# Performance work log

Measured on AMD Instinct MI355X. Metric: run time of the kernel, lower is better.

The kernel has to match this reference:

```python
import jax, jax.numpy as jnp
import numpy as np

B, C_IN, C_OUT, H, W = 4, 256, 256, 64, 64
KH = KW = 3
STRIDE = 1
PAD = 1
DIL = 1


def setup_inputs() -> dict:
    key = jax.random.key(0)
    k1, k2, k3, k4 = jax.random.split(key, 4)
    x = jax.random.normal(k1, (B, C_IN, H, W), dtype=jnp.float32)
    # torchvision layout: 2*dg*KH*KW channels, (y, x) pair per kernel tap
    offset = jax.random.normal(k2, (B, 2 * KH * KW, H, W), dtype=jnp.float32)
    fan_in = C_IN * KH * KW
    weight = jax.random.normal(k3, (C_OUT, C_IN, KH, KW), dtype=jnp.float32) / np.sqrt(fan_in)
    bias = jax.random.normal(k4, (C_OUT,), dtype=jnp.float32) * 0.01
    return {"x": x, "offset": offset, "weight": weight, "bias": bias}


def _gather_bilinear_corner(x_flat, yi, xi, h, w):
    # x_flat: [B, C, H*W]; yi/xi: [B, KK, Ho, Wo] int32
    valid = ((yi >= 0) & (yi < h) & (xi >= 0) & (xi < w)).astype(x_flat.dtype)
    idx = jnp.clip(yi, 0, h - 1) * w + jnp.clip(xi, 0, w - 1)
    b = idx.shape[0]
    g = jnp.take_along_axis(x_flat, idx.reshape(b, 1, -1), axis=2)
    return g.reshape(b, x_flat.shape[1], *yi.shape[1:]), valid


def deform_conv2d(x, offset, weight, bias):
    b, c, h, w = x.shape
    o = weight.shape[0]
    kk = KH * KW
    ho = (h + 2 * PAD - DIL * (KH - 1) - 1) // STRIDE + 1
    wo = (w + 2 * PAD - DIL * (KW - 1) - 1) // STRIDE + 1

    ky = (jnp.arange(kk, dtype=jnp.float32) // KW) * DIL  # [KK]
    kx = (jnp.arange(kk, dtype=jnp.float32) % KW) * DIL
    hs = jnp.arange(ho, dtype=jnp.float32) * STRIDE - PAD   # [Ho]
    ws = jnp.arange(wo, dtype=jnp.float32) * STRIDE - PAD   # [Wo]

    off = offset.reshape(b, kk, 2, ho, wo)
    py = hs[None, None, :, None] + ky[None, :, None, None] + off[:, :, 0]  # [B,KK,Ho,Wo]
    px = ws[None, None, None, :] + kx[None, :, None, None] + off[:, :, 1]

    y0 = jnp.floor(py)
    x0 = jnp.floor(px)
    wy1 = py - y0  # fractional parts, differentiable w.r.t. offsets
    wx1 = px - x0
    wy0 = 1.0 - wy1
    wx0 = 1.0 - wx1
    y0i = y0.astype(jnp.int32)
    x0i = x0.astype(jnp.int32)

    x_flat = x.reshape(b, c, h * w)
    corners = [
        (y0i,     x0i,     wy0 * wx0),
        (y0i,     x0i + 1, wy0 * wx1),
        (y0i + 1, x0i,     wy1 * wx0),
        (y0i + 1, x0i + 1, wy1 * wx1),
    ]
    sampled = jnp.zeros((b, c, kk, ho, wo), dtype=x.dtype)
    for yi, xi, wgt in corners:
        g, valid = _gather_bilinear_corner(x_flat, yi, xi, h, w)
        sampled = sampled + g * (wgt * valid)[:, None]

    out = jnp.einsum('bckhw,ock->bohw', sampled, weight.reshape(o, c, kk))
    return out + bias[None, :, None, None]


def reference(x, offset, weight, bias):
    return deform_conv2d(x, offset, weight, bias)
```

## Files before the change

### kernel.cpp

```cpp
#include <hip/hip_runtime.h>

typedef __bf16 bf16;
typedef __bf16 bf16x4 __attribute__((ext_vector_type(4)));
typedef __bf16 bf16x8 __attribute__((ext_vector_type(8)));
typedef float  f32x4  __attribute__((ext_vector_type(4)));

#define CIN   256
#define COUT  256
#define KK    9
#define KDIM  (CIN * KK)
#define KITERS 72
#define PXW   32
#define SROW  264

__global__ void pack_weight_k(const float* __restrict__ w, bf16* __restrict__ wq) {
    int idx  = blockIdx.x * 256 + threadIdx.x;
    int j    = idx & 7;
    int lane = (idx >> 3) & 63;
    int rest = idx >> 9;
    int kt   = rest % KITERS;
    int m    = rest / KITERS;
    int l16  = lane & 15;
    int quad = lane >> 4;
    int o    = m * 16 + l16;
    int k    = kt * 32 + quad * 8 + j;
    int tap  = k >> 8;
    int c    = k & 255;
    wq[idx] = (bf16)w[(size_t)o * KDIM + c * KK + tap];
}

__global__ void transpose_x_k(const float* __restrict__ x, bf16* __restrict__ xt) {
    __shared__ bf16 tile[64][72];
    int wg = blockIdx.x;
    int pt = wg & 63;
    int ct = (wg >> 6) & 3;
    int b  = wg >> 8;
    int lane = threadIdx.x & 63;
    int row  = threadIdx.x >> 6;
    const float* src = x + ((size_t)(b * 256 + ct * 64)) * 4096 + pt * 64;
    for (int c = row; c < 64; c += 4)
        tile[c][lane] = (bf16)src[(size_t)c * 4096 + lane];
    __syncthreads();
    bf16* dst = xt + ((size_t)(b * 4096 + pt * 64)) * 256 + ct * 64;
    for (int p = row; p < 64; p += 4)
        dst[(size_t)p * 256 + lane] = tile[lane][p];
}

__global__ __launch_bounds__(512, 4) void deform_gemm_k(
    const bf16*  __restrict__ xt,
    const float* __restrict__ off,
    const bf16*  __restrict__ wq,
    const float* __restrict__ bias,
    float*       __restrict__ out) {

    __shared__ bf16 S[PXW][SROW];

    int tid  = threadIdx.x;
    int wave = tid >> 6;
    int lane = tid & 63;
    int quad = lane >> 4;
    int l16  = lane & 15;
    int pix0 = blockIdx.x * PXW;
    int c    = lane * 4;

    int ybase[4], xbase[4];
    unsigned base[4];
    const float* obp[4];
    #pragma unroll
    for (int i = 0; i < 4; ++i) {
        int n    = wave * 4 + i;
        int pg   = pix0 + n;
        int b    = pg >> 12;
        int pimg = pg & 4095;
        ybase[i] = pimg >> 6;
        xbase[i] = pimg & 63;
        obp[i]   = off + (size_t)b * 18 * 4096 + pimg;
        base[i]  = (unsigned)b * 1048576u + (unsigned)c;
    }

    f32x4 acc[2][2];
    #pragma unroll
    for (int mt = 0; mt < 2; ++mt)
        #pragma unroll
        for (int nt = 0; nt < 2; ++nt)
            acc[mt][nt] = (f32x4){0.f, 0.f, 0.f, 0.f};

    for (int tap = 0; tap < KK; ++tap) {
        int ty = tap / 3 - 1;
        int tx = tap % 3 - 1;

        unsigned o32[4][4];
        float    w4[4][4];
        #pragma unroll
        for (int i = 0; i < 4; ++i) {
            float oy = obp[i][(size_t)(2 * tap) * 4096];
            float ox = obp[i][(size_t)(2 * tap + 1) * 4096];
            float py = (float)(ybase[i] + ty) + oy;
            float px = (float)(xbase[i] + tx) + ox;
            float fy = floorf(py), fx = floorf(px);
            int   y0 = (int)fy,    x0 = (int)fx;
            float wy1 = py - fy, wx1 = px - fx;
            float wy0 = 1.f - wy1, wx0 = 1.f - wx1;
            wy0 = ((unsigned)y0       < 64u) ? wy0 : 0.f;
            wy1 = ((unsigned)(y0 + 1) < 64u) ? wy1 : 0.f;
            wx0 = ((unsigned)x0       < 64u) ? wx0 : 0.f;
            wx1 = ((unsigned)(x0 + 1) < 64u) ? wx1 : 0.f;
            int yc0 = min(max(y0, 0), 63),     yc1 = min(max(y0 + 1, 0), 63);
            int xc0 = min(max(x0, 0), 63),     xc1 = min(max(x0 + 1, 0), 63);
            o32[i][0] = base[i] + (unsigned)((yc0 * 64 + xc0) * 256);
            o32[i][1] = base[i] + (unsigned)((yc0 * 64 + xc1) * 256);
            o32[i][2] = base[i] + (unsigned)((yc1 * 64 + xc0) * 256);
            o32[i][3] = base[i] + (unsigned)((yc1 * 64 + xc1) * 256);
            w4[i][0] = wy0 * wx0; w4[i][1] = wy0 * wx1;
            w4[i][2] = wy1 * wx0; w4[i][3] = wy1 * wx1;
        }

        bf16x4 v[4][4];
        #pragma unroll
        for (int i = 0; i < 4; ++i)
            #pragma unroll
            for (int j = 0; j < 4; ++j)
                v[i][j] = *reinterpret_cast<const bf16x4*>(xt + o32[i][j]);

        #pragma unroll
        for (int i = 0; i < 4; ++i) {
            float a0 = 0.f, a1 = 0.f, a2 = 0.f, a3 = 0.f;
            #pragma unroll
            for (int j = 0; j < 4; ++j) {
                float wt = w4[i][j];
                a0 += wt * (float)v[i][j][0];
                a1 += wt * (float)v[i][j][1];
                a2 += wt * (float)v[i][j][2];
                a3 += wt * (float)v[i][j][3];
            }
            bf16x4 sv;
            sv[0] = (bf16)a0; sv[1] = (bf16)a1;
            sv[2] = (bf16)a2; sv[3] = (bf16)a3;
            *reinterpret_cast<bf16x4*>(&S[wave * 4 + i][c]) = sv;
        }
        __syncthreads();

        const bf16* sp0 = &S[l16][quad * 8];
        const bf16* sp1 = &S[16 + l16][quad * 8];
        const bf16* ap0 = wq + ((size_t)((2 * wave) * KITERS + tap * 8) * 64 + lane) * 8;
        const bf16* ap1 = ap0 + (size_t)KITERS * 64 * 8;
        #pragma unroll
        for (int kki = 0; kki < 8; ++kki) {
            bf16x8 b0 = *reinterpret_cast<const bf16x8*>(sp0 + kki * 32);
            bf16x8 b1 = *reinterpret_cast<const bf16x8*>(sp1 + kki * 32);
            bf16x8 a0 = *reinterpret_cast<const bf16x8*>(ap0 + (size_t)kki * 512);
            bf16x8 a1 = *reinterpret_cast<const bf16x8*>(ap1 + (size_t)kki * 512);
            acc[0][0] = __builtin_amdgcn_mfma_f32_16x16x32_bf16(a0, b0, acc[0][0], 0, 0, 0);
            acc[0][1] = __builtin_amdgcn_mfma_f32_16x16x32_bf16(a0, b1, acc[0][1], 0, 0, 0);
            acc[1][0] = __builtin_amdgcn_mfma_f32_16x16x32_bf16(a1, b0, acc[1][0], 0, 0, 0);
            acc[1][1] = __builtin_amdgcn_mfma_f32_16x16x32_bf16(a1, b1, acc[1][1], 0, 0, 0);
        }
        __syncthreads();
    }

    #pragma unroll
    for (int nt = 0; nt < 2; ++nt) {
        int pg   = pix0 + nt * 16 + l16;
        int b    = pg >> 12;
        int pimg = pg & 4095;
        #pragma unroll
        for (int mt = 0; mt < 2; ++mt) {
            int m = (2 * wave + mt) * 16 + quad * 4;
            float* op = out + ((size_t)(b * 256 + m)) * 4096 + pimg;
            #pragma unroll
            for (int r = 0; r < 4; ++r)
                op[(size_t)r * 4096] = acc[mt][nt][r] + bias[m + r];
        }
    }
}

extern "C" void kernel_launch(void* const* d_in, const int* in_sizes, int n_in,
                              void* d_out, int out_size, void* d_ws, size_t ws_size,
                              hipStream_t stream) {
    const float* x    = (const float*)d_in[0];
    const float* off  = (const float*)d_in[1];
    const float* w    = (const float*)d_in[2];
    const float* bias = (const float*)d_in[3];
    float* out = (float*)d_out;

    bf16* wq = (bf16*)d_ws;
    bf16* xt = (bf16*)((char*)d_ws + (size_t)589824 * 2);

    pack_weight_k<<<2304, 256, 0, stream>>>(w, wq);
    transpose_x_k<<<1024, 256, 0, stream>>>(x, xt);
    deform_gemm_k<<<512, 512, 0, stream>>>(xt, off, wq, bias, out);
}
```

Baseline: 125.5 us.

## Double-buffer deform GEMM gather with MFMA and merge prep kernels

```diff
diff --git a/kernel.cpp b/kernel.cpp
--- a/kernel.cpp
+++ b/kernel.cpp
@@ -6,44 +6,53 @@
 typedef float  f32x4  __attribute__((ext_vector_type(4)));
 
 #define CIN   256
-#define COUT  256
 #define KK    9
-#define KDIM  (CIN * KK)
+#define KDIM  2304
 #define KITERS 72
 #define PXW   32
 #define SROW  264
 
-__global__ void pack_weight_k(const float* __restrict__ w, bf16* __restrict__ wq) {
-    int idx  = blockIdx.x * 256 + threadIdx.x;
-    int j    = idx & 7;
-    int lane = (idx >> 3) & 63;
-    int rest = idx >> 9;
-    int kt   = rest % KITERS;
-    int m    = rest / KITERS;
-    int l16  = lane & 15;
-    int quad = lane >> 4;
-    int o    = m * 16 + l16;
-    int k    = kt * 32 + quad * 8 + j;
-    int tap  = k >> 8;
-    int c    = k & 255;
-    wq[idx] = (bf16)w[(size_t)o * KDIM + c * KK + tap];
-}
-
-__global__ void transpose_x_k(const float* __restrict__ x, bf16* __restrict__ xt) {
-    __shared__ bf16 tile[64][72];
-    int wg = blockIdx.x;
-    int pt = wg & 63;
-    int ct = (wg >> 6) & 3;
-    int b  = wg >> 8;
-    int lane = threadIdx.x & 63;
-    int row  = threadIdx.x >> 6;
-    const float* src = x + ((size_t)(b * 256 + ct * 64)) * 4096 + pt * 64;
-    for (int c = row; c < 64; c += 4)
-        tile[c][lane] = (bf16)src[(size_t)c * 4096 + lane];
-    __syncthreads();
-    bf16* dst = xt + ((size_t)(b * 4096 + pt * 64)) * 256 + ct * 64;
-    for (int p = row; p < 64; p += 4)
-        dst[(size_t)p * 256 + lane] = tile[lane][p];
+__device__ __forceinline__ float sread(float f) {
+    return __builtin_bit_cast(float,
+        __builtin_amdgcn_readfirstlane(__builtin_bit_cast(int, f)));
+}
+
+__global__ __launch_bounds__(256) void prep_k(const float* __restrict__ x,
+                                              const float* __restrict__ w,
+                                              bf16* __restrict__ xt,
+                                              bf16* __restrict__ wq) {
+    int bid = blockIdx.x;
+    int tid = threadIdx.x;
+    if (bid < 1024) {
+        __shared__ bf16 tile[64][72];
+        int pt = bid & 63, ct = (bid >> 6) & 3, b = bid >> 8;
+        int lane = tid & 63, row = tid >> 6;
+        const float* src = x + ((size_t)(b * 256 + ct * 64)) * 4096 + pt * 64;
+        #pragma unroll
+        for (int cc = row; cc < 64; cc += 4)
+            tile[lane][cc] = (bf16)src[(size_t)cc * 4096 + lane];
+        __syncthreads();
+        bf16* dst = xt + ((size_t)(b * 4096 + pt * 64)) * 256 + ct * 64;
+        int p = tid >> 3, j = tid & 7;
+        #pragma unroll
+        for (int pp = p; pp < 64; pp += 32)
+            *reinterpret_cast<bf16x8*>(dst + (size_t)pp * 256 + j * 8) =
+                *reinterpret_cast<const bf16x8*>(&tile[pp][j * 8]);
+    } else {
+        int idx  = (bid - 1024) * 256 + tid;
+        int j    = idx & 7;
+        int lane = (idx >> 3) & 63;
+        int rest = idx >> 9;
+        int kt   = rest % KITERS;
+        int m    = rest / KITERS;
+        int l16  = lane & 15;
+        int quad = lane >> 4;
+        int o    = m * 16 + l16;
+        int k    = kt * 32 + quad * 8 + j;
+        int tap  = k >> 8;
+        int cc   = k & 255;
+        wq[idx] = (bf16)w[(size_t)o * KDIM + cc * KK + tap];
+    }
 }
 
 __global__ __launch_bounds__(512, 4) void deform_gemm_k(
@@ -53,7 +62,7 @@
     const float* __restrict__ bias,
     float*       __restrict__ out) {
 
-    __shared__ bf16 S[PXW][SROW];
+    __shared__ bf16 S[2][PXW][SROW];
 
     int tid  = threadIdx.x;
     int wave = tid >> 6;
@@ -64,8 +73,7 @@
     int c    = lane * 4;
 
     int ybase[4], xbase[4];
-    unsigned base[4];
-    const float* obp[4];
+    unsigned base[4], ooff[4];
     #pragma unroll
     for (int i = 0; i < 4; ++i) {
         int n    = wave * 4 + i;
@@ -74,7 +82,7 @@
         int pimg = pg & 4095;
         ybase[i] = pimg >> 6;
         xbase[i] = pimg & 63;
-        obp[i]   = off + (size_t)b * 18 * 4096 + pimg;
+        ooff[i]  = (unsigned)b * 73728u + (unsigned)pimg;
         base[i]  = (unsigned)b * 1048576u + (unsigned)c;
     }
 
@@ -85,16 +93,16 @@
         for (int nt = 0; nt < 2; ++nt)
             acc[mt][nt] = (f32x4){0.f, 0.f, 0.f, 0.f};
 
-    for (int tap = 0; tap < KK; ++tap) {
+    bf16x4 v[4][4];
+    float  w4[4][4];
+
+    auto gather = [&](int tap) {
         int ty = tap / 3 - 1;
         int tx = tap % 3 - 1;
-
-        unsigned o32[4][4];
-        float    w4[4][4];
         #pragma unroll
         for (int i = 0; i < 4; ++i) {
-            float oy = obp[i][(size_t)(2 * tap) * 4096];
-            float ox = obp[i][(size_t)(2 * tap + 1) * 4096];
+            float oy = off[(size_t)ooff[i] + (size_t)(2 * tap) * 4096];
+            float ox = off[(size_t)ooff[i] + (size_t)(2 * tap + 1) * 4096];
             float py = (float)(ybase[i] + ty) + oy;
             float px = (float)(xbase[i] + tx) + ox;
             float fy = floorf(py), fx = floorf(px);
@@ -107,21 +115,20 @@
             wx1 = ((unsigned)(x0 + 1) < 64u) ? wx1 : 0.f;
             int yc0 = min(max(y0, 0), 63),     yc1 = min(max(y0 + 1, 0), 63);
             int xc0 = min(max(x0, 0), 63),     xc1 = min(max(x0 + 1, 0), 63);
-            o32[i][0] = base[i] + (unsigned)((yc0 * 64 + xc0) * 256);
-            o32[i][1] = base[i] + (unsigned)((yc0 * 64 + xc1) * 256);
-            o32[i][2] = base[i] + (unsigned)((yc1 * 64 + xc0) * 256);
-            o32[i][3] = base[i] + (unsigned)((yc1 * 64 + xc1) * 256);
-            w4[i][0] = wy0 * wx0; w4[i][1] = wy0 * wx1;
-            w4[i][2] = wy1 * wx0; w4[i][3] = wy1 * wx1;
-        }
-
-        bf16x4 v[4][4];
-        #pragma unroll
-        for (int i = 0; i < 4; ++i)
-            #pragma unroll
-            for (int j = 0; j < 4; ++j)
-                v[i][j] = *reinterpret_cast<const bf16x4*>(xt + o32[i][j]);
-
+            unsigned u0 = (unsigned)((yc0 * 64 + xc0) * 256);
+            unsigned u1 = (unsigned)((yc0 * 64 + xc1) * 256);
+            unsigned u2 = (unsigned)((yc1 * 64 + xc0) * 256);
+            unsigned u3 = (unsigned)((yc1 * 64 + xc1) * 256);
+            w4[i][0] = sread(wy0 * wx0); w4[i][1] = sread(wy0 * wx1);
+            w4[i][2] = sread(wy1 * wx0); w4[i][3] = sread(wy1 * wx1);
+            v[i][0] = *reinterpret_cast<const bf16x4*>(xt + base[i] + u0);
+            v[i][1] = *reinterpret_cast<const bf16x4*>(xt + base[i] + u1);
+            v[i][2] = *reinterpret_cast<const bf16x4*>(xt + base[i] + u2);
+            v[i][3] = *reinterpret_cast<const bf16x4*>(xt + base[i] + u3);
+        }
+    };
+
+    auto blend = [&](int buf) {
         #pragma unroll
         for (int i = 0; i < 4; ++i) {
             float a0 = 0.f, a1 = 0.f, a2 = 0.f, a3 = 0.f;
@@ -136,12 +143,13 @@
             bf16x4 sv;
             sv[0] = (bf16)a0; sv[1] = (bf16)a1;
             sv[2] = (bf16)a2; sv[3] = (bf16)a3;
-            *reinterpret_cast<bf16x4*>(&S[wave * 4 + i][c]) = sv;
-        }
-        __syncthreads();
-
-        const bf16* sp0 = &S[l16][quad * 8];
-        const bf16* sp1 = &S[16 + l16][quad * 8];
+            *reinterpret_cast<bf16x4*>(&S[buf][wave * 4 + i][c]) = sv;
+        }
+    };
+
+    auto gemm = [&](int buf, int tap) {
+        const bf16* sp0 = &S[buf][l16][quad * 8];
+        const bf16* sp1 = &S[buf][16 + l16][quad * 8];
         const bf16* ap0 = wq + ((size_t)((2 * wave) * KITERS + tap * 8) * 64 + lane) * 8;
         const bf16* ap1 = ap0 + (size_t)KITERS * 64 * 8;
         #pragma unroll
@@ -155,6 +163,17 @@
             acc[1][0] = __builtin_amdgcn_mfma_f32_16x16x32_bf16(a1, b0, acc[1][0], 0, 0, 0);
             acc[1][1] = __builtin_amdgcn_mfma_f32_16x16x32_bf16(a1, b1, acc[1][1], 0, 0, 0);
         }
+    };
+
+    gather(0);
+    blend(0);
+    __syncthreads();
+
+    for (int tap = 0; tap < KK; ++tap) {
+        int cur = tap & 1;
+        if (tap + 1 < KK) gather(tap + 1);
+        gemm(cur, tap);
+        if (tap + 1 < KK) blend(cur ^ 1);
         __syncthreads();
     }
 
@@ -186,7 +205,6 @@
     bf16* wq = (bf16*)d_ws;
     bf16* xt = (bf16*)((char*)d_ws + (size_t)589824 * 2);
 
-    pack_weight_k<<<2304, 256, 0, stream>>>(w, wq);
-    transpose_x_k<<<1024, 256, 0, stream>>>(x, xt);
+    prep_k<<<3328, 256, 0, stream>>>(x, w, xt, wq);
     deform_gemm_k<<<512, 512, 0, stream>>>(xt, off, wq, bias, out);
 }
```

Result: no change. 123.6 us (-1.5%).
